# Kernel tuning notes

Measured on AMD Instinct MI355X. Metric: run time of the kernel, lower is better.

Reference implementation:

```python
import jax, jax.numpy as jnp
import numpy as np


def setup_inputs() -> dict:
    key = jax.random.key(0)
    k1, k2 = jax.random.split(key)
    src = jax.random.normal(k1, (16, 3, 1024, 1024), dtype=jnp.float32)
    dst = jax.random.normal(k2, (16, 3, 1024, 1024), dtype=jnp.float32)
    return {"src": src, "dst": dst}


def reference(src, dst):
    b, c, h, w = src.shape  # c == 3
    A = src.reshape(b, c, h * w)  # (b, 3, N)
    B = dst.reshape(b, c, h * w)
    Amean = jnp.mean(A, axis=-1, keepdims=True)  # (b, 3, 1)
    Bmean = jnp.mean(B, axis=-1, keepdims=True)
    Ac = A - Amean
    Bc = B - Bmean
    # covariance-like 3x3 matrices over the large spatial dim
    AAt = jnp.einsum('bin,bjn->bij', Ac, Ac)  # (b, 3, 3)
    BAt = jnp.einsum('bin,bjn->bij', Bc, Ac)
    AAt = AAt + 0.001 * jnp.eye(c, dtype=AAt.dtype)
    AAti = jnp.linalg.inv(AAt)
    x = jnp.einsum('bij,bjk->bik', BAt, AAti)  # (b, 3, 3)
    C = jnp.einsum('bij,bjn->bin', x, Ac) + Bmean  # (b, 3, N)
    return C.reshape(b, c, h, w)
```

## Files before the change

kernel.cpp:

```cpp
#include <hip/hip_runtime.h>

#define NPIX  (1024 * 1024)
#define NVEC  (NPIX / 4)
#define NSTAT 21
#define RBLOCKS  128
#define RTHREADS 256

__global__ __launch_bounds__(RTHREADS) void reduce_stats(
    const float4* __restrict__ src, const float4* __restrict__ dst,
    double* __restrict__ partials)
{
    const int b  = blockIdx.y;
    const int pb = blockIdx.x;

    const float4* A0 = src + (size_t)b * 3 * NVEC;
    const float4* A1 = A0 + NVEC;
    const float4* A2 = A0 + 2 * NVEC;
    const float4* B0 = dst + (size_t)b * 3 * NVEC;
    const float4* B1 = B0 + NVEC;
    const float4* B2 = B0 + 2 * NVEC;

    double acc[NSTAT];
#pragma unroll
    for (int s = 0; s < NSTAT; ++s) acc[s] = 0.0;

#define ACCUM(ax0, ax1, ax2, bx0, bx1, bx2)                                  \
    do {                                                                     \
        double A0d = (ax0), A1d = (ax1), A2d = (ax2);                        \
        double B0d = (bx0), B1d = (bx1), B2d = (bx2);                        \
        acc[0] += A0d;  acc[1] += A1d;  acc[2] += A2d;                       \
        acc[3] += B0d;  acc[4] += B1d;  acc[5] += B2d;                       \
        acc[6]  += A0d * A0d; acc[7]  += A0d * A1d; acc[8]  += A0d * A2d;    \
        acc[9]  += A1d * A1d; acc[10] += A1d * A2d; acc[11] += A2d * A2d;    \
        acc[12] += B0d * A0d; acc[13] += B0d * A1d; acc[14] += B0d * A2d;    \
        acc[15] += B1d * A0d; acc[16] += B1d * A1d; acc[17] += B1d * A2d;    \
        acc[18] += B2d * A0d; acc[19] += B2d * A1d; acc[20] += B2d * A2d;    \
    } while (0)

    const int stride = RBLOCKS * RTHREADS;
    for (int p = pb * RTHREADS + threadIdx.x; p < NVEC; p += stride) {
        float4 a0 = A0[p], a1 = A1[p], a2 = A2[p];
        float4 b0 = B0[p], b1 = B1[p], b2 = B2[p];
        ACCUM(a0.x, a1.x, a2.x, b0.x, b1.x, b2.x);
        ACCUM(a0.y, a1.y, a2.y, b0.y, b1.y, b2.y);
        ACCUM(a0.z, a1.z, a2.z, b0.z, b1.z, b2.z);
        ACCUM(a0.w, a1.w, a2.w, b0.w, b1.w, b2.w);
    }
#undef ACCUM

#pragma unroll
    for (int s = 0; s < NSTAT; ++s) {
        double v = acc[s];
        for (int off = 32; off > 0; off >>= 1) v += __shfl_down(v, off, 64);
        acc[s] = v;
    }

    __shared__ double part[RTHREADS / 64][NSTAT];
    const int lane = threadIdx.x & 63;
    const int wid  = threadIdx.x >> 6;
    if (lane == 0) {
#pragma unroll
        for (int s = 0; s < NSTAT; ++s) part[wid][s] = acc[s];
    }
    __syncthreads();

    if (threadIdx.x < NSTAT) {
        const int s = threadIdx.x;
        double v = part[0][s] + part[1][s] + part[2][s] + part[3][s];
        partials[((size_t)b * NSTAT + s) * RBLOCKS + pb] = v;
    }
}

__global__ __launch_bounds__(RBLOCKS) void solve3x3(
    const double* __restrict__ partials, float* __restrict__ coef)
{
    const int b = blockIdx.x;
    const int t = threadIdx.x;

    __shared__ double wsum[NSTAT][2];

#pragma unroll
    for (int s = 0; s < NSTAT; ++s) {
        double v = partials[((size_t)b * NSTAT + s) * RBLOCKS + t];
        for (int off = 32; off > 0; off >>= 1) v += __shfl_down(v, off, 64);
        if ((t & 63) == 0) wsum[s][t >> 6] = v;
    }
    __syncthreads();

    if (t == 0) {
        double st[NSTAT];
#pragma unroll
        for (int s = 0; s < NSTAT; ++s) st[s] = wsum[s][0] + wsum[s][1];

        const double N = (double)NPIX;
        double am[3] = {st[0] / N, st[1] / N, st[2] / N};
        double bm[3] = {st[3] / N, st[4] / N, st[5] / N};

        double AA[3][3];
        AA[0][0] = st[6]  - N * am[0] * am[0] + 0.001;
        AA[0][1] = st[7]  - N * am[0] * am[1];
        AA[0][2] = st[8]  - N * am[0] * am[2];
        AA[1][1] = st[9]  - N * am[1] * am[1] + 0.001;
        AA[1][2] = st[10] - N * am[1] * am[2];
        AA[2][2] = st[11] - N * am[2] * am[2] + 0.001;
        AA[1][0] = AA[0][1]; AA[2][0] = AA[0][2]; AA[2][1] = AA[1][2];

        double BA[3][3];
#pragma unroll
        for (int i = 0; i < 3; ++i)
#pragma unroll
            for (int j = 0; j < 3; ++j)
                BA[i][j] = st[12 + 3 * i + j] - N * bm[i] * am[j];

        double c00 =  AA[1][1] * AA[2][2] - AA[1][2] * AA[2][1];
        double c01 = -(AA[1][0] * AA[2][2] - AA[1][2] * AA[2][0]);
        double c02 =  AA[1][0] * AA[2][1] - AA[1][1] * AA[2][0];
        double det = AA[0][0] * c00 + AA[0][1] * c01 + AA[0][2] * c02;
        double id  = 1.0 / det;

        double inv[3][3];
        inv[0][0] = c00 * id;
        inv[1][0] = c01 * id;
        inv[2][0] = c02 * id;
        inv[0][1] = -(AA[0][1] * AA[2][2] - AA[0][2] * AA[2][1]) * id;
        inv[1][1] =  (AA[0][0] * AA[2][2] - AA[0][2] * AA[2][0]) * id;
        inv[2][1] = -(AA[0][0] * AA[2][1] - AA[0][1] * AA[2][0]) * id;
        inv[0][2] =  (AA[0][1] * AA[1][2] - AA[0][2] * AA[1][1]) * id;
        inv[1][2] = -(AA[0][0] * AA[1][2] - AA[0][2] * AA[1][0]) * id;
        inv[2][2] =  (AA[0][0] * AA[1][1] - AA[0][1] * AA[1][0]) * id;

        double X[3][3];
#pragma unroll
        for (int i = 0; i < 3; ++i)
#pragma unroll
            for (int j = 0; j < 3; ++j)
                X[i][j] = BA[i][0] * inv[0][j] + BA[i][1] * inv[1][j] +
                          BA[i][2] * inv[2][j];

        float* cb = coef + b * 12;
#pragma unroll
        for (int i = 0; i < 3; ++i) {
#pragma unroll
            for (int j = 0; j < 3; ++j) cb[3 * i + j] = (float)X[i][j];
            cb[9 + i] = (float)(bm[i] - (X[i][0] * am[0] + X[i][1] * am[1] +
                                         X[i][2] * am[2]));
        }
    }
}

__global__ __launch_bounds__(256) void apply_map(
    const float4* __restrict__ src, float4* __restrict__ out,
    const float* __restrict__ coef)
{
    const int b = blockIdx.y;
    const float* cb = coef + b * 12;
    const float x00 = cb[0], x01 = cb[1], x02 = cb[2];
    const float x10 = cb[3], x11 = cb[4], x12 = cb[5];
    const float x20 = cb[6], x21 = cb[7], x22 = cb[8];
    const float o0 = cb[9], o1 = cb[10], o2 = cb[11];

    const float4* A0 = src + (size_t)b * 3 * NVEC;
    const float4* A1 = A0 + NVEC;
    const float4* A2 = A0 + 2 * NVEC;
    float4* O0 = out + (size_t)b * 3 * NVEC;
    float4* O1 = O0 + NVEC;
    float4* O2 = O0 + 2 * NVEC;

    const int stride = gridDim.x * blockDim.x;
    for (int p = blockIdx.x * blockDim.x + threadIdx.x; p < NVEC; p += stride) {
        float4 a0 = A0[p], a1 = A1[p], a2 = A2[p];
        float4 r0, r1, r2;
#define LANE(L)                                                              \
        r0.L = fmaf(x00, a0.L, fmaf(x01, a1.L, fmaf(x02, a2.L, o0)));        \
        r1.L = fmaf(x10, a0.L, fmaf(x11, a1.L, fmaf(x12, a2.L, o1)));        \
        r2.L = fmaf(x20, a0.L, fmaf(x21, a1.L, fmaf(x22, a2.L, o2)));
        LANE(x) LANE(y) LANE(z) LANE(w)
#undef LANE
        O0[p] = r0; O1[p] = r1; O2[p] = r2;
    }
}

extern "C" void kernel_launch(void* const* d_in, const int* in_sizes, int n_in,
                              void* d_out, int out_size, void* d_ws, size_t ws_size,
                              hipStream_t stream)
{
    const float4* src = (const float4*)d_in[0];
    const float4* dst = (const float4*)d_in[1];
    float4* out = (float4*)d_out;

    const int batches = in_sizes[0] / (3 * NPIX);

    double* partials = (double*)d_ws;
    float*  coef = (float*)((char*)d_ws +
                            (size_t)batches * NSTAT * RBLOCKS * sizeof(double));

    reduce_stats<<<dim3(RBLOCKS, batches), RTHREADS, 0, stream>>>(src, dst, partials);
    solve3x3<<<batches, RBLOCKS, 0, stream>>>(partials, (float*)coef);
    apply_map<<<dim3(128, batches), 256, 0, stream>>>(src, out, coef);
}
```

Baseline: 509.8 us.

## Accumulate stats in fp32 and software-pipeline loads in reduce and apply kernels

```diff
diff --git a/kernel.cpp b/kernel.cpp
--- a/kernel.cpp
+++ b/kernel.cpp
@@ -5,8 +5,9 @@
 #define NSTAT 21
 #define RBLOCKS  128
 #define RTHREADS 256
-
-__global__ __launch_bounds__(RTHREADS) void reduce_stats(
+#define RITERS (NVEC / (RBLOCKS * RTHREADS))
+
+__global__ __launch_bounds__(RTHREADS, 4) void reduce_stats(
     const float4* __restrict__ src, const float4* __restrict__ dst,
     double* __restrict__ partials)
 {
@@ -20,39 +21,65 @@
     const float4* B1 = B0 + NVEC;
     const float4* B2 = B0 + 2 * NVEC;
 
-    double acc[NSTAT];
-#pragma unroll
-    for (int s = 0; s < NSTAT; ++s) acc[s] = 0.0;
-
-#define ACCUM(ax0, ax1, ax2, bx0, bx1, bx2)                                  \
+    float acc[NSTAT];
+#pragma unroll
+    for (int s = 0; s < NSTAT; ++s) acc[s] = 0.0f;
+
+#define ACC1(A0v, A1v, A2v, B0v, B1v, B2v)                                   \
     do {                                                                     \
-        double A0d = (ax0), A1d = (ax1), A2d = (ax2);                        \
-        double B0d = (bx0), B1d = (bx1), B2d = (bx2);                        \
-        acc[0] += A0d;  acc[1] += A1d;  acc[2] += A2d;                       \
-        acc[3] += B0d;  acc[4] += B1d;  acc[5] += B2d;                       \
-        acc[6]  += A0d * A0d; acc[7]  += A0d * A1d; acc[8]  += A0d * A2d;    \
-        acc[9]  += A1d * A1d; acc[10] += A1d * A2d; acc[11] += A2d * A2d;    \
-        acc[12] += B0d * A0d; acc[13] += B0d * A1d; acc[14] += B0d * A2d;    \
-        acc[15] += B1d * A0d; acc[16] += B1d * A1d; acc[17] += B1d * A2d;    \
-        acc[18] += B2d * A0d; acc[19] += B2d * A1d; acc[20] += B2d * A2d;    \
+        acc[0] += (A0v); acc[1] += (A1v); acc[2] += (A2v);                   \
+        acc[3] += (B0v); acc[4] += (B1v); acc[5] += (B2v);                   \
+        acc[6]  = fmaf((A0v), (A0v), acc[6]);                                \
+        acc[7]  = fmaf((A0v), (A1v), acc[7]);                                \
+        acc[8]  = fmaf((A0v), (A2v), acc[8]);                                \
+        acc[9]  = fmaf((A1v), (A1v), acc[9]);                                \
+        acc[10] = fmaf((A1v), (A2v), acc[10]);                               \
+        acc[11] = fmaf((A2v), (A2v), acc[11]);                               \
+        acc[12] = fmaf((B0v), (A0v), acc[12]);                               \
+        acc[13] = fmaf((B0v), (A1v), acc[13]);                               \
+        acc[14] = fmaf((B0v), (A2v), acc[14]);                               \
+        acc[15] = fmaf((B1v), (A0v), acc[15]);                               \
+        acc[16] = fmaf((B1v), (A1v), acc[16]);                               \
+        acc[17] = fmaf((B1v), (A2v), acc[17]);                               \
+        acc[18] = fmaf((B2v), (A0v), acc[18]);                               \
+        acc[19] = fmaf((B2v), (A1v), acc[19]);                               \
+        acc[20] = fmaf((B2v), (A2v), acc[20]);                               \
     } while (0)
 
+#define ACC4(a0, a1, a2, b0, b1, b2)                                         \
+    do {                                                                     \
+        ACC1(a0.x, a1.x, a2.x, b0.x, b1.x, b2.x);                            \
+        ACC1(a0.y, a1.y, a2.y, b0.y, b1.y, b2.y);                            \
+        ACC1(a0.z, a1.z, a2.z, b0.z, b1.z, b2.z);                            \
+        ACC1(a0.w, a1.w, a2.w, b0.w, b1.w, b2.w);                            \
+    } while (0)
+
     const int stride = RBLOCKS * RTHREADS;
-    for (int p = pb * RTHREADS + threadIdx.x; p < NVEC; p += stride) {
-        float4 a0 = A0[p], a1 = A1[p], a2 = A2[p];
-        float4 b0 = B0[p], b1 = B1[p], b2 = B2[p];
-        ACCUM(a0.x, a1.x, a2.x, b0.x, b1.x, b2.x);
-        ACCUM(a0.y, a1.y, a2.y, b0.y, b1.y, b2.y);
-        ACCUM(a0.z, a1.z, a2.z, b0.z, b1.z, b2.z);
-        ACCUM(a0.w, a1.w, a2.w, b0.w, b1.w, b2.w);
-    }
-#undef ACCUM
-
+    int p = pb * RTHREADS + threadIdx.x;
+
+    float4 a0 = A0[p], a1 = A1[p], a2 = A2[p];
+    float4 b0 = B0[p], b1 = B1[p], b2 = B2[p];
+
+#pragma unroll
+    for (int it = 0; it < RITERS - 1; ++it) {
+        const int pn = p + stride;
+        float4 na0 = A0[pn], na1 = A1[pn], na2 = A2[pn];
+        float4 nb0 = B0[pn], nb1 = B1[pn], nb2 = B2[pn];
+        ACC4(a0, a1, a2, b0, b1, b2);
+        a0 = na0; a1 = na1; a2 = na2;
+        b0 = nb0; b1 = nb1; b2 = nb2;
+        p = pn;
+    }
+    ACC4(a0, a1, a2, b0, b1, b2);
+#undef ACC4
+#undef ACC1
+
+    double accd[NSTAT];
 #pragma unroll
     for (int s = 0; s < NSTAT; ++s) {
-        double v = acc[s];
+        double v = (double)acc[s];
         for (int off = 32; off > 0; off >>= 1) v += __shfl_down(v, off, 64);
-        acc[s] = v;
+        accd[s] = v;
     }
 
     __shared__ double part[RTHREADS / 64][NSTAT];
@@ -60,7 +87,7 @@
     const int wid  = threadIdx.x >> 6;
     if (lane == 0) {
 #pragma unroll
-        for (int s = 0; s < NSTAT; ++s) part[wid][s] = acc[s];
+        for (int s = 0; s < NSTAT; ++s) part[wid][s] = accd[s];
     }
     __syncthreads();
 
@@ -148,7 +175,7 @@
     }
 }
 
-__global__ __launch_bounds__(256) void apply_map(
+__global__ __launch_bounds__(256, 4) void apply_map(
     const float4* __restrict__ src, float4* __restrict__ out,
     const float* __restrict__ coef)
 {
@@ -166,18 +193,38 @@
     float4* O1 = O0 + NVEC;
     float4* O2 = O0 + 2 * NVEC;
 
-    const int stride = gridDim.x * blockDim.x;
-    for (int p = blockIdx.x * blockDim.x + threadIdx.x; p < NVEC; p += stride) {
-        float4 a0 = A0[p], a1 = A1[p], a2 = A2[p];
-        float4 r0, r1, r2;
-#define LANE(L)                                                              \
-        r0.L = fmaf(x00, a0.L, fmaf(x01, a1.L, fmaf(x02, a2.L, o0)));        \
-        r1.L = fmaf(x10, a0.L, fmaf(x11, a1.L, fmaf(x12, a2.L, o1)));        \
-        r2.L = fmaf(x20, a0.L, fmaf(x21, a1.L, fmaf(x22, a2.L, o2)));
-        LANE(x) LANE(y) LANE(z) LANE(w)
-#undef LANE
-        O0[p] = r0; O1[p] = r1; O2[p] = r2;
-    }
+    const int stride = RBLOCKS * 256;
+    int p = blockIdx.x * 256 + threadIdx.x;
+
+#define APPLY_STORE(pp, a0, a1, a2)                                          \
+    do {                                                                     \
+        float4 r0, r1, r2;                                                   \
+        r0.x = fmaf(x00, a0.x, fmaf(x01, a1.x, fmaf(x02, a2.x, o0)));        \
+        r1.x = fmaf(x10, a0.x, fmaf(x11, a1.x, fmaf(x12, a2.x, o1)));        \
+        r2.x = fmaf(x20, a0.x, fmaf(x21, a1.x, fmaf(x22, a2.x, o2)));        \
+        r0.y = fmaf(x00, a0.y, fmaf(x01, a1.y, fmaf(x02, a2.y, o0)));        \
+        r1.y = fmaf(x10, a0.y, fmaf(x11, a1.y, fmaf(x12, a2.y, o1)));        \
+        r2.y = fmaf(x20, a0.y, fmaf(x21, a1.y, fmaf(x22, a2.y, o2)));        \
+        r0.z = fmaf(x00, a0.z, fmaf(x01, a1.z, fmaf(x02, a2.z, o0)));        \
+        r1.z = fmaf(x10, a0.z, fmaf(x11, a1.z, fmaf(x12, a2.z, o1)));        \
+        r2.z = fmaf(x20, a0.z, fmaf(x21, a1.z, fmaf(x22, a2.z, o2)));        \
+        r0.w = fmaf(x00, a0.w, fmaf(x01, a1.w, fmaf(x02, a2.w, o0)));        \
+        r1.w = fmaf(x10, a0.w, fmaf(x11, a1.w, fmaf(x12, a2.w, o1)));        \
+        r2.w = fmaf(x20, a0.w, fmaf(x21, a1.w, fmaf(x22, a2.w, o2)));        \
+        O0[pp] = r0; O1[pp] = r1; O2[pp] = r2;                               \
+    } while (0)
+
+    float4 a0 = A0[p], a1 = A1[p], a2 = A2[p];
+#pragma unroll
+    for (int it = 0; it < RITERS - 1; ++it) {
+        const int pn = p + stride;
+        float4 na0 = A0[pn], na1 = A1[pn], na2 = A2[pn];
+        APPLY_STORE(p, a0, a1, a2);
+        a0 = na0; a1 = na1; a2 = na2;
+        p = pn;
+    }
+    APPLY_STORE(p, a0, a1, a2);
+#undef APPLY_STORE
 }
 
 extern "C" void kernel_launch(void* const* d_in, const int* in_sizes, int n_in,
@@ -196,5 +243,5 @@
 
     reduce_stats<<<dim3(RBLOCKS, batches), RTHREADS, 0, stream>>>(src, dst, partials);
     solve3x3<<<batches, RBLOCKS, 0, stream>>>(partials, (float*)coef);
-    apply_map<<<dim3(128, batches), 256, 0, stream>>>(src, out, coef);
-}
+    apply_map<<<dim3(RBLOCKS, batches), 256, 0, stream>>>(src, out, coef);
+}
```

New measurement: 513.0 us. No clear change (+0.6%).
